# Kernel optimization log

Measured on AMD Instinct MI355X. Metric: run time of the kernel, lower is better.

The kernel has to match this reference:

```python
import jax, jax.numpy as jnp
import numpy as np

SIZE = 256
D_IN = 256
EPS = 1e-3  # keras BatchNormalization default epsilon


def _mlp(x, W1, b1, W2, b2):
    # smallMLP: Dense(size, relu) -> Dense(size)
    return jax.nn.relu(x @ W1 + b1) @ W2 + b2


def setup_inputs() -> dict:
    key = jax.random.key(0)
    ks = jax.random.split(key, 20)
    B, L1, L2 = 16, 1024, 1024
    s = 0.02
    inp = {
        "seq1M": jax.random.normal(ks[0], (B, L1, D_IN), jnp.float32),
        "seq2M": jax.random.normal(ks[1], (B, L2, D_IN), jnp.float32),
        "distogram": jax.random.uniform(ks[2], (B, L1, L2), jnp.float32),
        # shared K/Q/V smallMLP params (same layers applied to seq1 and seq2)
        "kW1": jax.random.normal(ks[3], (D_IN, SIZE), jnp.float32) * s,
        "kb1": jnp.zeros((SIZE,), jnp.float32),
        "kW2": jax.random.normal(ks[4], (SIZE, SIZE), jnp.float32) * s,
        "kb2": jnp.zeros((SIZE,), jnp.float32),
        "qW1": jax.random.normal(ks[5], (D_IN, SIZE), jnp.float32) * s,
        "qb1": jnp.zeros((SIZE,), jnp.float32),
        "qW2": jax.random.normal(ks[6], (SIZE, SIZE), jnp.float32) * s,
        "qb2": jnp.zeros((SIZE,), jnp.float32),
        "vW1": jax.random.normal(ks[7], (D_IN, SIZE), jnp.float32) * s,
        "vb1": jnp.zeros((SIZE,), jnp.float32),
        "vW2": jax.random.normal(ks[8], (SIZE, SIZE), jnp.float32) * s,
        "vb2": jnp.zeros((SIZE,), jnp.float32),
        # output projections
        "fc1W": jax.random.normal(ks[9], (SIZE, SIZE), jnp.float32) * s,
        "fc1b": jnp.zeros((SIZE,), jnp.float32),
        "fc2W": jax.random.normal(ks[10], (SIZE, SIZE), jnp.float32) * s,
        "fc2b": jnp.zeros((SIZE,), jnp.float32),
        # shared BatchNorm (inference mode, moving stats)
        "bn_gamma": jnp.ones((SIZE,), jnp.float32),
        "bn_beta": jnp.zeros((SIZE,), jnp.float32),
        "bn_mean": jnp.zeros((SIZE,), jnp.float32),
        "bn_var": jnp.ones((SIZE,), jnp.float32),
    }
    return inp


def reference(seq1M, seq2M, distogram,
              kW1, kb1, kW2, kb2,
              qW1, qb1, qW2, qb2,
              vW1, vb1, vW2, vb2,
              fc1W, fc1b, fc2W, fc2b,
              bn_gamma, bn_beta, bn_mean, bn_var):
    size = jnp.float32(SIZE)
    k1 = _mlp(seq1M, kW1, kb1, kW2, kb2)   # [B, L1, S]
    q1 = _mlp(seq1M, qW1, qb1, qW2, qb2)
    v1 = _mlp(seq1M, vW1, vb1, vW2, vb2)
    k2 = _mlp(seq2M, kW1, kb1, kW2, kb2)   # [B, L2, S]
    q2 = _mlp(seq2M, qW1, qb1, qW2, qb2)
    v2 = _mlp(seq2M, vW1, vb1, vW2, vb2)

    # distogram-scaled scores, softmax over axis 1 (query axis — non-standard)
    scores1 = jnp.einsum('bls,bms->blm', q1, k2) * distogram / size  # [B, L1, L2]
    w1 = jax.nn.softmax(scores1, axis=1)
    scores2 = jnp.einsum('bms,bls->bml', q2, k1) * jnp.transpose(distogram, (0, 2, 1)) / size  # [B, L2, L1]
    w2 = jax.nn.softmax(scores2, axis=1)

    # transpose(matmul(V^T, W), [0,2,1]) == einsum contracting the softmax axis
    ap1 = jnp.einsum('bls,blm->bms', v1, w1)  # [B, L2, S]
    ap2 = jnp.einsum('bms,bml->bls', v2, w2)  # [B, L1, S]

    def bn(x):
        return (x - bn_mean) * jax.lax.rsqrt(bn_var + EPS) * bn_gamma + bn_beta

    out1 = bn(jax.nn.relu(ap1 @ fc1W + fc1b))
    out2 = bn(jax.nn.relu(ap2 @ fc2W + fc2b))
    return out1, out2
```

## Files before the change

kernel.cpp:

```cpp
#include <hip/hip_runtime.h>
#include <hip/hip_bf16.h>


typedef __attribute__((ext_vector_type(8))) short bf16x8;
typedef __attribute__((ext_vector_type(4))) float f32x4;
typedef unsigned short u16;

__device__ __forceinline__ unsigned int f2bfbits(float f) {
  union { float f; unsigned int i; } v; v.f = f;
  return (v.i + 0x7fffu + ((v.i >> 16) & 1u)) >> 16;
}
__device__ __forceinline__ unsigned int pk2(float a, float b) {
  return f2bfbits(a) | (f2bfbits(b) << 16);
}
__device__ __forceinline__ float bf2f(u16 x) {
  union { unsigned int i; float f; } v;
  v.i = (unsigned int)x << 16;
  return v.f;
}

__global__ void pack_wt(const float* __restrict__ w0, const float* __restrict__ w1,
                        const float* __restrict__ w2, const float* __restrict__ w3,
                        const float* __restrict__ w4, const float* __restrict__ w5,
                        const float* __restrict__ w6, const float* __restrict__ w7,
                        u16* __restrict__ out) {
  const float* wsel[8] = {w0, w1, w2, w3, w4, w5, w6, w7};
  const float* W = wsel[blockIdx.y];
  u16* o = out + (size_t)blockIdx.y * 65536;
  int i0 = blockIdx.x * 1024 + threadIdx.x * 4;
  int n = i0 >> 8, k = i0 & 255;
  float a = W[(k + 0) * 256 + n];
  float b = W[(k + 1) * 256 + n];
  float c = W[(k + 2) * 256 + n];
  float d = W[(k + 3) * 256 + n];
  uint2 pv;
  pv.x = pk2(a, b);
  pv.y = pk2(c, d);
  *(uint2*)(o + i0) = pv;
}

__global__ __launch_bounds__(256)
void pack_disto(const float* __restrict__ D, u16* __restrict__ Dt) {
  __shared__ u16 T[64][72];
  const int b = blockIdx.z, l0 = blockIdx.y * 64, m0 = blockIdx.x * 64;
  const float* src = D + (size_t)b * (1024 * 1024);
  u16* dst = Dt + (size_t)b * (1024 * 1024);
  const int r = threadIdx.x >> 2, c0 = (threadIdx.x & 3) * 16;
  float4 f[4];
#pragma unroll
  for (int q = 0; q < 4; ++q)
    f[q] = *(const float4*)(src + (size_t)(l0 + r) * 1024 + m0 + c0 + q * 4);
  uint4 p0, p1;
  p0.x = pk2(f[0].x, f[0].y); p0.y = pk2(f[0].z, f[0].w);
  p0.z = pk2(f[1].x, f[1].y); p0.w = pk2(f[1].z, f[1].w);
  p1.x = pk2(f[2].x, f[2].y); p1.y = pk2(f[2].z, f[2].w);
  p1.z = pk2(f[3].x, f[3].y); p1.w = pk2(f[3].z, f[3].w);
  *(uint4*)&T[r][c0] = p0;
  *(uint4*)&T[r][c0 + 8] = p1;
  __syncthreads();
  u16 vals[16];
#pragma unroll
  for (int k = 0; k < 16; ++k) vals[k] = T[c0 + k][r];
  *(uint4*)(dst + (size_t)(m0 + r) * 1024 + l0 + c0) = *(uint4*)&vals[0];
  *(uint4*)(dst + (size_t)(m0 + r) * 1024 + l0 + c0 + 8) = *(uint4*)&vals[8];
}

__global__ __launch_bounds__(256, 2)
void mlp3_fused(const float* __restrict__ seqA, const float* __restrict__ seqB,
                const u16* __restrict__ Wt8,
                const float* __restrict__ kb1, const float* __restrict__ kb2,
                const float* __restrict__ qb1, const float* __restrict__ qb2,
                const float* __restrict__ vb1, const float* __restrict__ vb2,
                u16* __restrict__ kA, u16* __restrict__ qA, u16* __restrict__ vA,
                u16* __restrict__ kB, u16* __restrict__ qB, u16* __restrict__ vB)
{
  __shared__ u16 As[64][256];
  __shared__ u16 Hl[64][256];

  const int tid = threadIdx.x;
  const int lane = tid & 63;
  const int w = tid >> 6;
  const int l15 = lane & 15, lq = lane >> 4;
  const int seqsel = blockIdx.x >> 8;
  const size_t m0 = (size_t)(blockIdx.x & 255) * 64;
  const float* __restrict__ seq = seqsel ? seqB : seqA;

  {
    const int row = tid >> 2, cg = tid & 3;
    const float* src = seq + (m0 + row) * 256 + cg * 64;
#pragma unroll
    for (int cc = 0; cc < 8; ++cc) {
      float4 f0 = *(const float4*)(src + cc * 8);
      float4 f1 = *(const float4*)(src + cc * 8 + 4);
      uint4 pk;
      pk.x = pk2(f0.x, f0.y);
      pk.y = pk2(f0.z, f0.w);
      pk.z = pk2(f1.x, f1.y);
      pk.w = pk2(f1.z, f1.w);
      const int ch = (cg * 8 + cc) ^ (row & 7);
      *(uint4*)&As[row][ch * 8] = pk;
    }
  }
  __syncthreads();

#pragma unroll
  for (int mlp = 0; mlp < 3; ++mlp) {
    const u16* __restrict__ W1 = Wt8 + (size_t)(mlp * 2) * 65536;
    const u16* __restrict__ W2 = Wt8 + (size_t)(mlp * 2 + 1) * 65536;
    const float* __restrict__ b1 = (mlp == 0) ? kb1 : (mlp == 1) ? qb1 : vb1;
    const float* __restrict__ b2 = (mlp == 0) ? kb2 : (mlp == 1) ? qb2 : vb2;
    u16* __restrict__ dst =
        (mlp == 0) ? (seqsel ? kB : kA) : (mlp == 1) ? (seqsel ? qB : qA) : (seqsel ? vB : vA);

    float b1v[4][4];
#pragma unroll
    for (int ni = 0; ni < 4; ++ni)
#pragma unroll
      for (int r = 0; r < 4; ++r) b1v[ni][r] = b1[w * 64 + ni * 16 + 4 * lq + r];
    float b2v[4];
#pragma unroll
    for (int ni = 0; ni < 4; ++ni) b2v[ni] = b2[w * 64 + ni * 16 + l15];

    f32x4 a1[4][4];
#pragma unroll
    for (int ni = 0; ni < 4; ++ni)
#pragma unroll
      for (int mj = 0; mj < 4; ++mj) a1[ni][mj] = (f32x4)0.0f;
#pragma unroll
    for (int ks = 0; ks < 8; ++ks) {
      bf16x8 wf[4], af[4];
#pragma unroll
      for (int ni = 0; ni < 4; ++ni)
        wf[ni] = *(const bf16x8*)(W1 + (size_t)(w * 64 + ni * 16 + l15) * 256 + ks * 32 + lq * 8);
#pragma unroll
      for (int mj = 0; mj < 4; ++mj) {
        const int row = mj * 16 + l15;
        const int ch = (ks * 4 + lq) ^ (row & 7);
        af[mj] = *(const bf16x8*)&As[row][ch * 8];
      }
#pragma unroll
      for (int ni = 0; ni < 4; ++ni)
#pragma unroll
        for (int mj = 0; mj < 4; ++mj)
          a1[ni][mj] = __builtin_amdgcn_mfma_f32_16x16x32_bf16(wf[ni], af[mj], a1[ni][mj], 0, 0, 0);
    }

    __syncthreads();
#pragma unroll
    for (int ni = 0; ni < 4; ++ni) {
      const int chl = w * 8 + ni * 2 + (lq >> 1);
#pragma unroll
      for (int mj = 0; mj < 4; ++mj) {
        const int m = mj * 16 + l15;
        float h0 = fmaxf(a1[ni][mj][0] + b1v[ni][0], 0.f);
        float h1 = fmaxf(a1[ni][mj][1] + b1v[ni][1], 0.f);
        float h2 = fmaxf(a1[ni][mj][2] + b1v[ni][2], 0.f);
        float h3 = fmaxf(a1[ni][mj][3] + b1v[ni][3], 0.f);
        uint2 pv;
        pv.x = pk2(h0, h1);
        pv.y = pk2(h2, h3);
        const int ch = chl ^ (m & 7);
        *(uint2*)&Hl[m][ch * 8 + (lq & 1) * 4] = pv;
      }
    }
    __syncthreads();

    f32x4 a2[4][4];
#pragma unroll
    for (int mi = 0; mi < 4; ++mi)
#pragma unroll
      for (int ni = 0; ni < 4; ++ni) a2[mi][ni] = (f32x4)0.0f;
#pragma unroll
    for (int ks = 0; ks < 8; ++ks) {
      bf16x8 wf[4], hf[4];
#pragma unroll
      for (int ni = 0; ni < 4; ++ni)
        wf[ni] = *(const bf16x8*)(W2 + (size_t)(w * 64 + ni * 16 + l15) * 256 + ks * 32 + lq * 8);
#pragma unroll
      for (int mi = 0; mi < 4; ++mi) {
        const int row = mi * 16 + l15;
        const int ch = (ks * 4 + lq) ^ (row & 7);
        hf[mi] = *(const bf16x8*)&Hl[row][ch * 8];
      }
#pragma unroll
      for (int mi = 0; mi < 4; ++mi)
#pragma unroll
        for (int ni = 0; ni < 4; ++ni)
          a2[mi][ni] = __builtin_amdgcn_mfma_f32_16x16x32_bf16(hf[mi], wf[ni], a2[mi][ni], 0, 0, 0);
    }

#pragma unroll
    for (int ni = 0; ni < 4; ++ni) {
      const int col = w * 64 + ni * 16 + l15;
      const float bb = b2v[ni];
#pragma unroll
      for (int mi = 0; mi < 4; ++mi) {
        const size_t grow0 = m0 + mi * 16 + 4 * lq;
        float z[4];
#pragma unroll
        for (int r = 0; r < 4; ++r) z[r] = a2[mi][ni][r] + bb;
        if (mlp != 2) {
#pragma unroll
          for (int r = 0; r < 4; ++r)
            dst[(grow0 + r) * 256 + col] = (u16)f2bfbits(z[r]);
        } else {
          uint2 pv;
          pv.x = pk2(z[0], z[1]);
          pv.y = pk2(z[2], z[3]);
          const size_t bb2 = grow0 >> 10, lrow = grow0 & 1023;
          *(uint2*)(dst + ((size_t)bb2 * 256 + col) * 1024 + lrow) = pv;
        }
      }
    }
  }
}

enum { EPI_RELU_BF16 = 0, EPI_BF16 = 1, EPI_VT = 2, EPI_BN = 3 };

template <bool AF32, int EPI>
__global__ __launch_bounds__(256, 2)
void gemm_mfma(const void* __restrict__ Aptr, const u16* __restrict__ Wt,
               const float* __restrict__ bias, void* __restrict__ Cout,
               const float* __restrict__ bn_g, const float* __restrict__ bn_b,
               const float* __restrict__ bn_m, const float* __restrict__ bn_v)
{
  __shared__ u16 As[128][64];
  __shared__ u16 Ws[64][64];
  const int tid = threadIdx.x;
  const int lane = tid & 63;
  const int w = tid >> 6;
  const int wr = w >> 1, wc = w & 1;
  const int l15 = lane & 15, lq = lane >> 4;
  const size_t bm = (size_t)blockIdx.x * 128;
  const int bn = blockIdx.y * 64;

  const int sar = tid >> 1, sah = tid & 1;
  const int swr = tid >> 2, swc = tid & 3;

  f32x4 acc[4][2];
#pragma unroll
  for (int mi = 0; mi < 4; ++mi)
#pragma unroll
    for (int ni = 0; ni < 2; ++ni) acc[mi][ni] = (f32x4)0.0f;

  for (int k0 = 0; k0 < 256; k0 += 64) {
    __syncthreads();
    if (AF32) {
      const float* A = (const float*)Aptr + (bm + sar) * 256 + k0 + sah * 32;
#pragma unroll
      for (int c = 0; c < 4; ++c) {
        float4 f0 = *(const float4*)(A + c * 8);
        float4 f1 = *(const float4*)(A + c * 8 + 4);
        uint4 pk;
        pk.x = pk2(f0.x, f0.y);
        pk.y = pk2(f0.z, f0.w);
        pk.z = pk2(f1.x, f1.y);
        pk.w = pk2(f1.z, f1.w);
        int cc = (sah * 4 + c) ^ (sar & 7);
        *(uint4*)&As[sar][cc * 8] = pk;
      }
    } else {
      const u16* A = (const u16*)Aptr + (bm + sar) * 256 + k0 + sah * 32;
#pragma unroll
      for (int c = 0; c < 4; ++c) {
        uint4 v = *(const uint4*)(A + c * 8);
        int cc = (sah * 4 + c) ^ (sar & 7);
        *(uint4*)&As[sar][cc * 8] = v;
      }
    }
    {
      const u16* Wp = Wt + (size_t)(bn + swr) * 256 + k0 + swc * 16;
#pragma unroll
      for (int c = 0; c < 2; ++c) {
        uint4 v = *(const uint4*)(Wp + c * 8);
        int cc = (swc * 2 + c) ^ (swr & 7);
        *(uint4*)&Ws[swr][cc * 8] = v;
      }
    }
    __syncthreads();
#pragma unroll
    for (int ks = 0; ks < 2; ++ks) {
      bf16x8 af[4], wf[2];
#pragma unroll
      for (int mi = 0; mi < 4; ++mi) {
        int row = wr * 64 + mi * 16 + l15;
        int cc = (ks * 4 + lq) ^ (row & 7);
        af[mi] = *(const bf16x8*)&As[row][cc * 8];
      }
#pragma unroll
      for (int ni = 0; ni < 2; ++ni) {
        int row = wc * 32 + ni * 16 + l15;
        int cc = (ks * 4 + lq) ^ (row & 7);
        wf[ni] = *(const bf16x8*)&Ws[row][cc * 8];
      }
#pragma unroll
      for (int mi = 0; mi < 4; ++mi)
#pragma unroll
        for (int ni = 0; ni < 2; ++ni)
          acc[mi][ni] = __builtin_amdgcn_mfma_f32_16x16x32_bf16(
              af[mi], wf[ni], acc[mi][ni], 0, 0, 0);
    }
  }

#pragma unroll
  for (int ni = 0; ni < 2; ++ni) {
    const int col = bn + wc * 32 + ni * 16 + l15;
    const float bi = bias[col];
    float g = 0.f, be = 0.f, mu = 0.f, iv = 0.f;
    if (EPI == EPI_BN) {
      g = bn_g[col];
      be = bn_b[col];
      mu = bn_m[col];
      iv = rsqrtf(bn_v[col] + 1e-3f);
    }
#pragma unroll
    for (int mi = 0; mi < 4; ++mi) {
      const size_t grow0 = bm + wr * 64 + mi * 16 + 4 * lq;
      float z[4];
#pragma unroll
      for (int r = 0; r < 4; ++r) z[r] = acc[mi][ni][r] + bi;
      if (EPI == EPI_RELU_BF16) {
#pragma unroll
        for (int r = 0; r < 4; ++r)
          ((u16*)Cout)[(grow0 + r) * 256 + col] = (u16)f2bfbits(fmaxf(z[r], 0.f));
      } else if (EPI == EPI_BF16) {
#pragma unroll
        for (int r = 0; r < 4; ++r)
          ((u16*)Cout)[(grow0 + r) * 256 + col] = (u16)f2bfbits(z[r]);
      } else if (EPI == EPI_VT) {
        uint2 pv;
        pv.x = pk2(z[0], z[1]);
        pv.y = pk2(z[2], z[3]);
        const size_t b = grow0 >> 10, lrow = grow0 & 1023;
        *(uint2*)((u16*)Cout + ((size_t)b * 256 + col) * 1024 + lrow) = pv;
      } else {
#pragma unroll
        for (int r = 0; r < 4; ++r) {
          float zz = fmaxf(z[r], 0.f);
          ((float*)Cout)[(grow0 + r) * 256 + col] = (zz - mu) * iv * g + be;
        }
      }
    }
  }
}

__global__ __launch_bounds__(256, 2)
void attn_mfma(const u16* __restrict__ Qa, const u16* __restrict__ Ka,
               const u16* __restrict__ Va, u16* __restrict__ OutA,
               const u16* __restrict__ Qb, const u16* __restrict__ Kb,
               const u16* __restrict__ Vb, u16* __restrict__ OutB,
               const u16* __restrict__ D1t, const float* __restrict__ D2)
{
  __shared__ union U {
    struct {
      u16 Ks[2][32][256];
      u16 Vts[2][256][32];
      u16 Pl[64][40];
    } s;
    u16 Osw[4][16][264];
  } u;

  const int orig = blockIdx.x;
  const int lid = (orig & 7) * 64 + (orig >> 3);
  const int dir = lid >> 8;
  const int b = (lid >> 4) & 15;
  const int i0 = (lid & 15) * 64;

  const u16* __restrict__ Q = dir ? Qb : Qa;
  const u16* __restrict__ K = dir ? Kb : Ka;
  const u16* __restrict__ Vt = dir ? Vb : Va;
  u16* __restrict__ Out = dir ? OutB : OutA;

  const int tid = threadIdx.x;
  const int lane = tid & 63;
  const int w = tid >> 6;
  const int l15 = lane & 15, lq = lane >> 4;
  const size_t sbase = (size_t)b * (1024 * 256);
  const size_t vtbase = (size_t)b * (256 * 1024);
  const size_t dbase = (size_t)b * (1024 * 1024);

  bf16x8 q[8];
  {
    const u16* Qp = Q + sbase + (size_t)(i0 + w * 16 + l15) * 256 + lq * 8;
#pragma unroll
    for (int ks = 0; ks < 8; ++ks) q[ks] = *(const bf16x8*)(Qp + ks * 32);
  }

  const int cb0 = w * 4;
  auto stage = [&](int bi, int j0) {
#pragma unroll
    for (int i = 0; i < 4; ++i) {
      const int cb = cb0 + i;
      {
        const int krow = cb * 2 + (lane >> 5);
        const int kch = (lane & 31) ^ (krow & 7);
        const u16* gs = K + sbase + (size_t)(j0 + krow) * 256 + kch * 8;
        __builtin_amdgcn_global_load_lds(
            (const __attribute__((address_space(1))) unsigned int*)gs,
            (__attribute__((address_space(3))) unsigned int*)&u.s.Ks[bi][cb * 2][0],
            16, 0, 0);
      }
      {
        const int vrow = cb * 16 + (lane >> 2);
        const int vch = lane & 3;
        const u16* gs = Vt + vtbase + (size_t)vrow * 1024 + j0 + ((vch ^ (vrow & 3)) * 8);
        __builtin_amdgcn_global_load_lds(
            (const __attribute__((address_space(1))) unsigned int*)gs,
            (__attribute__((address_space(3))) unsigned int*)&u.s.Vts[bi][cb * 16][0],
            16, 0, 0);
      }
    }
  };

  float mrow[4], lrow[4];
  f32x4 o[16];
#pragma unroll
  for (int r = 0; r < 4; ++r) { mrow[r] = -1e30f; lrow[r] = 0.f; }
#pragma unroll
  for (int nt = 0; nt < 16; ++nt) o[nt] = (f32x4)0.0f;

  stage(0, 0);

  const int vcc = lq ^ (l15 & 3);

  for (int t = 0; t < 32; ++t) {
    const int bi = t & 1;
    const int j0 = t * 32;

    u16 bregu[8];
    float bregf[8];
    if (dir == 0) {
#pragma unroll
      for (int nt = 0; nt < 2; ++nt)
#pragma unroll
        for (int r = 0; r < 4; ++r) {
          const size_t idx =
              dbase + (size_t)(i0 + w * 16 + 4 * lq + r) * 1024 + j0 + l15 + 16 * nt;
          bregu[nt * 4 + r] = D1t[idx];
        }
    } else {
#pragma unroll
      for (int nt = 0; nt < 2; ++nt)
#pragma unroll
        for (int r = 0; r < 4; ++r) {
          const size_t idx =
              dbase + (size_t)(i0 + w * 16 + 4 * lq + r) * 1024 + j0 + l15 + 16 * nt;
          bregf[nt * 4 + r] = D2[idx];
        }
    }

    if (t + 1 < 32) {
      stage(bi ^ 1, j0 + 32);
      asm volatile("s_waitcnt vmcnt(16)" ::: "memory");
    } else {
      asm volatile("s_waitcnt vmcnt(0)" ::: "memory");
    }
    __builtin_amdgcn_s_barrier();
    __builtin_amdgcn_sched_barrier(0);

    f32x4 sa[2];
    sa[0] = (f32x4)0.0f;
    sa[1] = (f32x4)0.0f;
#pragma unroll
    for (int ks = 0; ks < 8; ++ks)
#pragma unroll
      for (int nt = 0; nt < 2; ++nt) {
        const int row = nt * 16 + l15;
        const int cc = (ks * 4 + lq) ^ (row & 7);
        bf16x8 kb = *(const bf16x8*)&u.s.Ks[bi][row][cc * 8];
        sa[nt] = __builtin_amdgcn_mfma_f32_16x16x32_bf16(q[ks], kb, sa[nt], 0, 0, 0);
      }

    float sc[4], p0v[4], p1v[4];
#pragma unroll
    for (int r = 0; r < 4; ++r) {
      float b0, b1;
      if (dir == 0) {
        b0 = bf2f(bregu[r]);
        b1 = bf2f(bregu[4 + r]);
      } else {
        b0 = bregf[r];
        b1 = bregf[4 + r];
      }
      float s0 = sa[0][r] * b0 * 0.00390625f;
      float s1 = sa[1][r] * b1 * 0.00390625f;
      float mx = fmaxf(s0, s1);
      mx = fmaxf(mx, __shfl_xor(mx, 1, 16));
      mx = fmaxf(mx, __shfl_xor(mx, 2, 16));
      mx = fmaxf(mx, __shfl_xor(mx, 4, 16));
      mx = fmaxf(mx, __shfl_xor(mx, 8, 16));
      const float mn = fmaxf(mrow[r], mx);
      const float scr = __expf(mrow[r] - mn);
      const float p0 = __expf(s0 - mn);
      const float p1 = __expf(s1 - mn);
      float rs = p0 + p1;
      rs += __shfl_xor(rs, 1, 16);
      rs += __shfl_xor(rs, 2, 16);
      rs += __shfl_xor(rs, 4, 16);
      rs += __shfl_xor(rs, 8, 16);
      lrow[r] = lrow[r] * scr + rs;
      mrow[r] = mn;
      sc[r] = scr;
      p0v[r] = p0;
      p1v[r] = p1;
    }
#pragma unroll
    for (int r = 0; r < 4; ++r) {
      const int qrow = w * 16 + 4 * lq + r;
      u.s.Pl[qrow][l15] = (u16)f2bfbits(p0v[r]);
      u.s.Pl[qrow][16 + l15] = (u16)f2bfbits(p1v[r]);
    }
#pragma unroll
    for (int nt = 0; nt < 16; ++nt) {
#pragma unroll
      for (int r = 0; r < 4; ++r) o[nt][r] *= sc[r];
    }
    __threadfence_block();
    const bf16x8 pa = *(const bf16x8*)&u.s.Pl[w * 16 + l15][lq * 8];
#pragma unroll
    for (int nt = 0; nt < 16; ++nt) {
      bf16x8 vb = *(const bf16x8*)&u.s.Vts[bi][nt * 16 + l15][vcc * 8];
      o[nt] = __builtin_amdgcn_mfma_f32_16x16x32_bf16(pa, vb, o[nt], 0, 0, 0);
    }

    asm volatile("s_waitcnt lgkmcnt(0)" ::: "memory");
    __builtin_amdgcn_s_barrier();
  }

  float inv[4];
#pragma unroll
  for (int r = 0; r < 4; ++r) inv[r] = 1.0f / lrow[r];
#pragma unroll
  for (int nt = 0; nt < 16; ++nt) {
#pragma unroll
    for (int r = 0; r < 4; ++r)
      u.Osw[w][4 * lq + r][nt * 16 + l15] = (u16)f2bfbits(o[nt][r] * inv[r]);
  }
  __threadfence_block();
  {
    const int orow = lane >> 2, och = (lane & 3) * 64;
    const u16* src = &u.Osw[w][orow][och];
    u16* dst = Out + sbase + (size_t)(i0 + w * 16 + orow) * 256 + och;
#pragma unroll
    for (int c = 0; c < 8; ++c) *(uint4*)(dst + c * 8) = *(const uint4*)(src + c * 8);
  }
}

extern "C" void kernel_launch(void* const* d_in, const int* in_sizes, int n_in,
                              void* d_out, int out_size, void* d_ws, size_t ws_size,
                              hipStream_t stream)
{
  (void)in_sizes; (void)n_in; (void)out_size; (void)ws_size;

  const float* seq1  = (const float*)d_in[0];
  const float* seq2  = (const float*)d_in[1];
  const float* disto = (const float*)d_in[2];
  const float* kW1 = (const float*)d_in[3];
  const float* kb1 = (const float*)d_in[4];
  const float* kW2 = (const float*)d_in[5];
  const float* kb2 = (const float*)d_in[6];
  const float* qW1 = (const float*)d_in[7];
  const float* qb1 = (const float*)d_in[8];
  const float* qW2 = (const float*)d_in[9];
  const float* qb2 = (const float*)d_in[10];
  const float* vW1 = (const float*)d_in[11];
  const float* vb1 = (const float*)d_in[12];
  const float* vW2 = (const float*)d_in[13];
  const float* vb2 = (const float*)d_in[14];
  const float* fc1W = (const float*)d_in[15];
  const float* fc1b = (const float*)d_in[16];
  const float* fc2W = (const float*)d_in[17];
  const float* fc2b = (const float*)d_in[18];
  const float* bn_g = (const float*)d_in[19];
  const float* bn_b = (const float*)d_in[20];
  const float* bn_m = (const float*)d_in[21];
  const float* bn_v = (const float*)d_in[22];

  char* ws = (char*)d_ws;
  const size_t MB = 1024 * 1024;
  u16* Wt8 = (u16*)(ws);
  u16* k1  = (u16*)(ws + 1 * MB);
  u16* q1  = (u16*)(ws + 9 * MB);
  u16* k2  = (u16*)(ws + 17 * MB);
  u16* q2  = (u16*)(ws + 25 * MB);
  u16* v1t = (u16*)(ws + 33 * MB);
  u16* v2t = (u16*)(ws + 41 * MB);
  u16* ap1 = (u16*)(ws + 49 * MB);
  u16* ap2 = (u16*)(ws + 57 * MB);
  u16* D1t = (u16*)(ws + 65 * MB);

  pack_wt<<<dim3(64, 8), 256, 0, stream>>>(kW1, kW2, qW1, qW2, vW1, vW2, fc1W, fc2W, Wt8);
  pack_disto<<<dim3(16, 16, 16), 256, 0, stream>>>(disto, D1t);

  mlp3_fused<<<dim3(512), dim3(256), 0, stream>>>(
      seq1, seq2, Wt8, kb1, kb2, qb1, qb2, vb1, vb2,
      k1, q1, v1t, k2, q2, v2t);

  attn_mfma<<<dim3(512), dim3(256), 0, stream>>>(
      k2, q1, v1t, ap1,
      k1, q2, v2t, ap2,
      D1t, disto);

  float* out1 = (float*)d_out;
  float* out2 = (float*)d_out + 4194304;
  dim3 ggrid(128, 4), gblk(256);
  gemm_mfma<false, EPI_BN><<<ggrid, gblk, 0, stream>>>(
      ap1, Wt8 + 6ull * 65536, fc1b, (void*)out1, bn_g, bn_b, bn_m, bn_v);
  gemm_mfma<false, EPI_BN><<<ggrid, gblk, 0, stream>>>(
      ap2, Wt8 + 7ull * 65536, fc2b, (void*)out2, bn_g, bn_b, bn_m, bn_v);
}
```

Measured before the change: 188.5 us.

## Drop distogram transpose pass, load V from global, lazy softmax rescale

Removes the pack_disto kernel, so direction 0 now reads the fp32 distogram with transposed (strided) indexing straight from global memory instead of a pre-transposed bf16 copy. V tiles are no longer staged in LDS; each lane loads its V fragments directly from global memory, which shrinks shared memory and allows raising launch bounds to 3 blocks per SIMD. The online softmax only rescales the accumulators when a new score exceeds the running max by a threshold, and the row-sum reduction across lanes is deferred to the end. The trade-off is uncoalesced strided distogram reads in dir 0 and global-latency V loads inside the loop, in exchange for skipping a separate pass over the full distogram.

```diff
diff --git a/kernel.cpp b/kernel.cpp
--- a/kernel.cpp
+++ b/kernel.cpp
@@ -12,11 +12,6 @@
 }
 __device__ __forceinline__ unsigned int pk2(float a, float b) {
   return f2bfbits(a) | (f2bfbits(b) << 16);
-}
-__device__ __forceinline__ float bf2f(u16 x) {
-  union { unsigned int i; float f; } v;
-  v.i = (unsigned int)x << 16;
-  return v.f;
 }
 
 __global__ void pack_wt(const float* __restrict__ w0, const float* __restrict__ w1,
@@ -39,32 +34,6 @@
   *(uint2*)(o + i0) = pv;
 }
 
-__global__ __launch_bounds__(256)
-void pack_disto(const float* __restrict__ D, u16* __restrict__ Dt) {
-  __shared__ u16 T[64][72];
-  const int b = blockIdx.z, l0 = blockIdx.y * 64, m0 = blockIdx.x * 64;
-  const float* src = D + (size_t)b * (1024 * 1024);
-  u16* dst = Dt + (size_t)b * (1024 * 1024);
-  const int r = threadIdx.x >> 2, c0 = (threadIdx.x & 3) * 16;
-  float4 f[4];
-#pragma unroll
-  for (int q = 0; q < 4; ++q)
-    f[q] = *(const float4*)(src + (size_t)(l0 + r) * 1024 + m0 + c0 + q * 4);
-  uint4 p0, p1;
-  p0.x = pk2(f[0].x, f[0].y); p0.y = pk2(f[0].z, f[0].w);
-  p0.z = pk2(f[1].x, f[1].y); p0.w = pk2(f[1].z, f[1].w);
-  p1.x = pk2(f[2].x, f[2].y); p1.y = pk2(f[2].z, f[2].w);
-  p1.z = pk2(f[3].x, f[3].y); p1.w = pk2(f[3].z, f[3].w);
-  *(uint4*)&T[r][c0] = p0;
-  *(uint4*)&T[r][c0 + 8] = p1;
-  __syncthreads();
-  u16 vals[16];
-#pragma unroll
-  for (int k = 0; k < 16; ++k) vals[k] = T[c0 + k][r];
-  *(uint4*)(dst + (size_t)(m0 + r) * 1024 + l0 + c0) = *(uint4*)&vals[0];
-  *(uint4*)(dst + (size_t)(m0 + r) * 1024 + l0 + c0 + 8) = *(uint4*)&vals[8];
-}
-
 __global__ __launch_bounds__(256, 2)
 void mlp3_fused(const float* __restrict__ seqA, const float* __restrict__ seqB,
                 const u16* __restrict__ Wt8,
@@ -344,17 +313,16 @@
   }
 }
 
-__global__ __launch_bounds__(256, 2)
+__global__ __launch_bounds__(256, 3)
 void attn_mfma(const u16* __restrict__ Qa, const u16* __restrict__ Ka,
                const u16* __restrict__ Va, u16* __restrict__ OutA,
                const u16* __restrict__ Qb, const u16* __restrict__ Kb,
                const u16* __restrict__ Vb, u16* __restrict__ OutB,
-               const u16* __restrict__ D1t, const float* __restrict__ D2)
+               const float* __restrict__ D2)
 {
   __shared__ union U {
     struct {
       u16 Ks[2][32][256];
-      u16 Vts[2][256][32];
       u16 Pl[64][40];
     } s;
     u16 Osw[4][16][264];
@@ -391,67 +359,51 @@
 #pragma unroll
     for (int i = 0; i < 4; ++i) {
       const int cb = cb0 + i;
-      {
-        const int krow = cb * 2 + (lane >> 5);
-        const int kch = (lane & 31) ^ (krow & 7);
-        const u16* gs = K + sbase + (size_t)(j0 + krow) * 256 + kch * 8;
-        __builtin_amdgcn_global_load_lds(
-            (const __attribute__((address_space(1))) unsigned int*)gs,
-            (__attribute__((address_space(3))) unsigned int*)&u.s.Ks[bi][cb * 2][0],
-            16, 0, 0);
-      }
-      {
-        const int vrow = cb * 16 + (lane >> 2);
-        const int vch = lane & 3;
-        const u16* gs = Vt + vtbase + (size_t)vrow * 1024 + j0 + ((vch ^ (vrow & 3)) * 8);
-        __builtin_amdgcn_global_load_lds(
-            (const __attribute__((address_space(1))) unsigned int*)gs,
-            (__attribute__((address_space(3))) unsigned int*)&u.s.Vts[bi][cb * 16][0],
-            16, 0, 0);
-      }
+      const int krow = cb * 2 + (lane >> 5);
+      const int kch = (lane & 31) ^ (krow & 7);
+      const u16* gs = K + sbase + (size_t)(j0 + krow) * 256 + kch * 8;
+      __builtin_amdgcn_global_load_lds(
+          (const __attribute__((address_space(1))) unsigned int*)gs,
+          (__attribute__((address_space(3))) unsigned int*)&u.s.Ks[bi][cb * 2][0],
+          16, 0, 0);
     }
   };
 
-  float mrow[4], lrow[4];
+  float mrow[4], lsum[4];
   f32x4 o[16];
 #pragma unroll
-  for (int r = 0; r < 4; ++r) { mrow[r] = -1e30f; lrow[r] = 0.f; }
+  for (int r = 0; r < 4; ++r) { mrow[r] = -1e30f; lsum[r] = 0.f; }
 #pragma unroll
   for (int nt = 0; nt < 16; ++nt) o[nt] = (f32x4)0.0f;
 
   stage(0, 0);
 
-  const int vcc = lq ^ (l15 & 3);
+  const u16* Vrow = Vt + vtbase + (size_t)l15 * 1024 + lq * 8;
 
   for (int t = 0; t < 32; ++t) {
     const int bi = t & 1;
     const int j0 = t * 32;
 
-    u16 bregu[8];
-    float bregf[8];
+    float breg[8];
     if (dir == 0) {
 #pragma unroll
       for (int nt = 0; nt < 2; ++nt)
 #pragma unroll
-        for (int r = 0; r < 4; ++r) {
-          const size_t idx =
-              dbase + (size_t)(i0 + w * 16 + 4 * lq + r) * 1024 + j0 + l15 + 16 * nt;
-          bregu[nt * 4 + r] = D1t[idx];
-        }
+        for (int r = 0; r < 4; ++r)
+          breg[nt * 4 + r] =
+              D2[dbase + (size_t)(j0 + l15 + 16 * nt) * 1024 + (i0 + w * 16 + 4 * lq + r)];
     } else {
 #pragma unroll
       for (int nt = 0; nt < 2; ++nt)
 #pragma unroll
-        for (int r = 0; r < 4; ++r) {
-          const size_t idx =
-              dbase + (size_t)(i0 + w * 16 + 4 * lq + r) * 1024 + j0 + l15 + 16 * nt;
-          bregf[nt * 4 + r] = D2[idx];
-        }
+        for (int r = 0; r < 4; ++r)
+          breg[nt * 4 + r] =
+              D2[dbase + (size_t)(i0 + w * 16 + 4 * lq + r) * 1024 + j0 + l15 + 16 * nt];
     }
 
     if (t + 1 < 32) {
       stage(bi ^ 1, j0 + 32);
-      asm volatile("s_waitcnt vmcnt(16)" ::: "memory");
+      asm volatile("s_waitcnt vmcnt(4)" ::: "memory");
     } else {
       asm volatile("s_waitcnt vmcnt(0)" ::: "memory");
     }
@@ -471,38 +423,41 @@
         sa[nt] = __builtin_amdgcn_mfma_f32_16x16x32_bf16(q[ks], kb, sa[nt], 0, 0, 0);
       }
 
-    float sc[4], p0v[4], p1v[4];
+    bf16x8 vf[8];
+#pragma unroll
+    for (int n2 = 0; n2 < 8; ++n2)
+      vf[n2] = *(const bf16x8*)(Vrow + (size_t)(n2 * 16) * 1024 + j0);
+
+    float s0[4], s1[4];
+    bool need = false;
 #pragma unroll
     for (int r = 0; r < 4; ++r) {
-      float b0, b1;
-      if (dir == 0) {
-        b0 = bf2f(bregu[r]);
-        b1 = bf2f(bregu[4 + r]);
-      } else {
-        b0 = bregf[r];
-        b1 = bregf[4 + r];
-      }
-      float s0 = sa[0][r] * b0 * 0.00390625f;
-      float s1 = sa[1][r] * b1 * 0.00390625f;
-      float mx = fmaxf(s0, s1);
-      mx = fmaxf(mx, __shfl_xor(mx, 1, 16));
-      mx = fmaxf(mx, __shfl_xor(mx, 2, 16));
-      mx = fmaxf(mx, __shfl_xor(mx, 4, 16));
-      mx = fmaxf(mx, __shfl_xor(mx, 8, 16));
-      const float mn = fmaxf(mrow[r], mx);
-      const float scr = __expf(mrow[r] - mn);
-      const float p0 = __expf(s0 - mn);
-      const float p1 = __expf(s1 - mn);
-      float rs = p0 + p1;
-      rs += __shfl_xor(rs, 1, 16);
-      rs += __shfl_xor(rs, 2, 16);
-      rs += __shfl_xor(rs, 4, 16);
-      rs += __shfl_xor(rs, 8, 16);
-      lrow[r] = lrow[r] * scr + rs;
-      mrow[r] = mn;
-      sc[r] = scr;
-      p0v[r] = p0;
-      p1v[r] = p1;
+      s0[r] = sa[0][r] * breg[r] * 0.00390625f;
+      s1[r] = sa[1][r] * breg[4 + r] * 0.00390625f;
+      need = need || (s0[r] > mrow[r] + 8.f) || (s1[r] > mrow[r] + 8.f);
+    }
+    if (__any(need)) {
+#pragma unroll
+      for (int r = 0; r < 4; ++r) {
+        float mx = fmaxf(s0[r], s1[r]);
+        mx = fmaxf(mx, __shfl_xor(mx, 1, 16));
+        mx = fmaxf(mx, __shfl_xor(mx, 2, 16));
+        mx = fmaxf(mx, __shfl_xor(mx, 4, 16));
+        mx = fmaxf(mx, __shfl_xor(mx, 8, 16));
+        const float mn = fmaxf(mrow[r], mx);
+        const float sc = __expf(mrow[r] - mn);
+        mrow[r] = mn;
+        lsum[r] *= sc;
+#pragma unroll
+        for (int nt = 0; nt < 16; ++nt) o[nt][r] *= sc;
+      }
+    }
+    float p0v[4], p1v[4];
+#pragma unroll
+    for (int r = 0; r < 4; ++r) {
+      p0v[r] = __expf(s0[r] - mrow[r]);
+      p1v[r] = __expf(s1[r] - mrow[r]);
+      lsum[r] += p0v[r] + p1v[r];
     }
 #pragma unroll
     for (int r = 0; r < 4; ++r) {
@@ -510,18 +465,18 @@
       u.s.Pl[qrow][l15] = (u16)f2bfbits(p0v[r]);
       u.s.Pl[qrow][16 + l15] = (u16)f2bfbits(p1v[r]);
     }
-#pragma unroll
-    for (int nt = 0; nt < 16; ++nt) {
-#pragma unroll
-      for (int r = 0; r < 4; ++r) o[nt][r] *= sc[r];
-    }
     __threadfence_block();
     const bf16x8 pa = *(const bf16x8*)&u.s.Pl[w * 16 + l15][lq * 8];
-#pragma unroll
-    for (int nt = 0; nt < 16; ++nt) {
-      bf16x8 vb = *(const bf16x8*)&u.s.Vts[bi][nt * 16 + l15][vcc * 8];
-      o[nt] = __builtin_amdgcn_mfma_f32_16x16x32_bf16(pa, vb, o[nt], 0, 0, 0);
-    }
+
+#pragma unroll
+    for (int nt = 0; nt < 8; ++nt)
+      o[nt] = __builtin_amdgcn_mfma_f32_16x16x32_bf16(pa, vf[nt], o[nt], 0, 0, 0);
+#pragma unroll
+    for (int n2 = 0; n2 < 8; ++n2)
+      vf[n2] = *(const bf16x8*)(Vrow + (size_t)((n2 + 8) * 16) * 1024 + j0);
+#pragma unroll
+    for (int nt = 0; nt < 8; ++nt)
+      o[nt + 8] = __builtin_amdgcn_mfma_f32_16x16x32_bf16(pa, vf[nt], o[nt + 8], 0, 0, 0);
 
     asm volatile("s_waitcnt lgkmcnt(0)" ::: "memory");
     __builtin_amdgcn_s_barrier();
@@ -529,7 +484,14 @@
 
   float inv[4];
 #pragma unroll
-  for (int r = 0; r < 4; ++r) inv[r] = 1.0f / lrow[r];
+  for (int r = 0; r < 4; ++r) {
+    float rs = lsum[r];
+    rs += __shfl_xor(rs, 1, 16);
+    rs += __shfl_xor(rs, 2, 16);
+    rs += __shfl_xor(rs, 4, 16);
+    rs += __shfl_xor(rs, 8, 16);
+    inv[r] = 1.0f / rs;
+  }
 #pragma unroll
   for (int nt = 0; nt < 16; ++nt) {
 #pragma unroll
@@ -587,10 +549,8 @@
   u16* v2t = (u16*)(ws + 41 * MB);
   u16* ap1 = (u16*)(ws + 49 * MB);
   u16* ap2 = (u16*)(ws + 57 * MB);
-  u16* D1t = (u16*)(ws + 65 * MB);
 
   pack_wt<<<dim3(64, 8), 256, 0, stream>>>(kW1, kW2, qW1, qW2, vW1, vW2, fc1W, fc2W, Wt8);
-  pack_disto<<<dim3(16, 16, 16), 256, 0, stream>>>(disto, D1t);
 
   mlp3_fused<<<dim3(512), dim3(256), 0, stream>>>(
       seq1, seq2, Wt8, kb1, kb2, qb1, qb2, vb1, vb2,
@@ -599,7 +559,7 @@
   attn_mfma<<<dim3(512), dim3(256), 0, stream>>>(
       k2, q1, v1t, ap1,
       k1, q2, v2t, ap2,
-      D1t, disto);
+      disto);
 
   float* out1 = (float*)d_out;
   float* out2 = (float*)d_out + 4194304;
```

Result: slower. 344.2 us (+82.6%).
